# Kernel tuning notes

Hardware: AMD Instinct MI355X
Metric: run time of the kernel (lower is better)

The kernel has to match this reference:

```python
import jax, jax.numpy as jnp
import numpy as np

B, S, E = 4, 2048, 1024
H, D = 16, 64
SCALE = D ** -0.5


def setup_inputs() -> dict:
    key = jax.random.key(0)
    ks = jax.random.split(key, 6)
    x = jax.random.normal(ks[0], (B, S, E), dtype=jnp.float32)
    # per-head projection weights stacked along head axis: [H, E, D]
    Wq = jax.random.normal(ks[1], (H, E, D), dtype=jnp.float32) * 0.02
    Wk = jax.random.normal(ks[2], (H, E, D), dtype=jnp.float32) * 0.02
    Wv = jax.random.normal(ks[3], (H, E, D), dtype=jnp.float32) * 0.02
    # output projection: concat(H*D) -> E, with bias (nn.Linear default)
    Wo = jax.random.normal(ks[4], (H * D, E), dtype=jnp.float32) * 0.02
    bo = jax.random.normal(ks[5], (E,), dtype=jnp.float32) * 0.02
    return {"x": x, "Wq": Wq, "Wk": Wk, "Wv": Wv, "Wo": Wo, "bo": bo}


def reference(x, Wq, Wk, Wv, Wo, bo):
    # batched QKV projections for all heads at once
    q = jnp.einsum('bse,hed->bhsd', x, Wq)
    k = jnp.einsum('bse,hed->bhsd', x, Wk)
    v = jnp.einsum('bse,hed->bhsd', x, Wv)
    # full (non-causal) attention, scores [b,h,s,s]
    scores = jnp.einsum('bhsd,bhtd->bhst', q, k) * SCALE
    attn = jax.nn.softmax(scores, axis=-1)
    o = jnp.einsum('bhst,bhtd->bhsd', attn, v)
    # concat heads in head order along feature dim -> [b,s,H*D]
    o = o.transpose(0, 2, 1, 3).reshape(x.shape[0], x.shape[1], -1)
    return o @ Wo + bo
```

## Files before the change

kernel.cpp:

```cpp
#include <hip/hip_runtime.h>
#include <hip/hip_fp16.h>
#include <stdint.h>

#define BB 4
#define SS 2048
#define EE 1024
#define HH 16
#define DD 64

typedef _Float16 half8 __attribute__((ext_vector_type(8)));
typedef __fp16 fp16x2 __attribute__((ext_vector_type(2)));
typedef float f32x4 __attribute__((ext_vector_type(4)));
typedef float f32x16 __attribute__((ext_vector_type(16)));
typedef uint32_t u32;
typedef uint32_t u32x2 __attribute__((ext_vector_type(2)));

#define MFMA32(a, b, c) __builtin_amdgcn_mfma_f32_16x16x32_f16((a), (b), (c), 0, 0, 0)
#define MFMA3216(a, b, c) __builtin_amdgcn_mfma_f32_32x32x16_f16((a), (b), (c), 0, 0, 0)

#define GLD_LDS16(g, l)                                                        \
  __builtin_amdgcn_global_load_lds(                                            \
      (const __attribute__((address_space(1))) u32*)(const void*)(g),          \
      (__attribute__((address_space(3))) u32*)(void*)(l), 16, 0, 0)

static __device__ __forceinline__ u32 pkh(float a, float b) {
  union { fp16x2 h; u32 u; } z;
  z.h = __builtin_amdgcn_cvt_pkrtz(a, b);
  return z.u;
}

static __device__ __forceinline__ void plswap(u32& a, u32& b) {
  asm("v_permlane32_swap_b32 %0, %1" : "+v"(a), "+v"(b));
}

__global__ __launch_bounds__(256) void conv_x_k(const float* __restrict__ x,
                                                _Float16* __restrict__ xh) {
  size_t i = ((size_t)blockIdx.x * 256 + threadIdx.x) * 8;
  f32x4 a = *(const f32x4*)(x + i);
  f32x4 b = *(const f32x4*)(x + i + 4);
  half8 o;
  o[0] = (_Float16)a[0]; o[1] = (_Float16)a[1];
  o[2] = (_Float16)a[2]; o[3] = (_Float16)a[3];
  o[4] = (_Float16)b[0]; o[5] = (_Float16)b[1];
  o[6] = (_Float16)b[2]; o[7] = (_Float16)b[3];
  *(half8*)(xh + i) = o;
}

__global__ __launch_bounds__(256) void conv_w_k(const float* __restrict__ Wq,
                                                const float* __restrict__ Wk,
                                                const float* __restrict__ Wv,
                                                _Float16* __restrict__ Wt) {
  __shared__ float T[64][65];
  int bid = blockIdx.x;
  int sel = bid >> 8, rem = bid & 255;
  int h = rem >> 4, e0 = (rem & 15) * 64;
  const float* W = (sel == 0 ? Wq : sel == 1 ? Wk : Wv) + (size_t)h * EE * DD;
  float scale = (sel == 0) ? 0.18033688011112042f : 1.0f;
  int tid = threadIdx.x;
  {
    int e = tid >> 2, d0 = (tid & 3) * 16;
#pragma unroll
    for (int i = 0; i < 4; ++i) {
      f32x4 v = *(const f32x4*)(W + (size_t)(e0 + e) * DD + d0 + i * 4);
      T[e][d0 + i * 4 + 0] = v[0];
      T[e][d0 + i * 4 + 1] = v[1];
      T[e][d0 + i * 4 + 2] = v[2];
      T[e][d0 + i * 4 + 3] = v[3];
    }
  }
  __syncthreads();
  {
    int d = tid >> 2, c0 = (tid & 3) * 16;
    half8 o0, o1;
#pragma unroll
    for (int i = 0; i < 8; ++i) o0[i] = (_Float16)(T[c0 + i][d] * scale);
#pragma unroll
    for (int i = 0; i < 8; ++i) o1[i] = (_Float16)(T[c0 + 8 + i][d] * scale);
    _Float16* dst = Wt + ((size_t)sel * 1024 + h * 64 + d) * EE + e0 + c0;
    *(half8*)dst = o0;
    *(half8*)(dst + 8) = o1;
  }
}

__global__ __launch_bounds__(256) void conv_wo_k(const float* __restrict__ Wo,
                                                 _Float16* __restrict__ Wot) {
  __shared__ float T[64][65];
  int bid = blockIdx.x;
  int k0 = (bid >> 4) * 64, n0 = (bid & 15) * 64;
  int tid = threadIdx.x;
  {
    int k = tid >> 2, c0 = (tid & 3) * 16;
#pragma unroll
    for (int i = 0; i < 4; ++i) {
      f32x4 v = *(const f32x4*)(Wo + (size_t)(k0 + k) * EE + n0 + c0 + i * 4);
      T[k][c0 + i * 4 + 0] = v[0];
      T[k][c0 + i * 4 + 1] = v[1];
      T[k][c0 + i * 4 + 2] = v[2];
      T[k][c0 + i * 4 + 3] = v[3];
    }
  }
  __syncthreads();
  {
    int n = tid >> 2, c0 = (tid & 3) * 16;
    half8 o0, o1;
#pragma unroll
    for (int i = 0; i < 8; ++i) o0[i] = (_Float16)T[c0 + i][n];
#pragma unroll
    for (int i = 0; i < 8; ++i) o1[i] = (_Float16)T[c0 + 8 + i][n];
    _Float16* dst = Wot + (size_t)(n0 + n) * EE + k0 + c0;
    *(half8*)dst = o0;
    *(half8*)(dst + 8) = o1;
  }
}

__global__ __launch_bounds__(256) void vtrans_k(const _Float16* __restrict__ v,
                                                _Float16* __restrict__ vT) {
  __shared__ _Float16 T[64][72];
  int bid = blockIdx.x;
  int bh = bid >> 5, st = bid & 31;
  const _Float16* vp = v + (size_t)bh * SS * DD + (size_t)st * 64 * DD;
  _Float16* op = vT + (size_t)bh * DD * SS + (size_t)st * 64;
  int tid = threadIdx.x;
  {
    int r = tid >> 2, c0 = (tid & 3) * 16;
    half8 a = *(const half8*)(vp + (size_t)r * DD + c0);
    half8 b = *(const half8*)(vp + (size_t)r * DD + c0 + 8);
#pragma unroll
    for (int j = 0; j < 8; ++j) T[c0 + j][r] = a[j];
#pragma unroll
    for (int j = 0; j < 8; ++j) T[c0 + 8 + j][r] = b[j];
  }
  __syncthreads();
  {
    int d = tid >> 2, sc = (tid & 3) * 16;
    half8 o0 = *(const half8*)&T[d][sc];
    half8 o1 = *(const half8*)&T[d][sc + 8];
    *(half8*)(op + (size_t)d * SS + sc) = o0;
    *(half8*)(op + (size_t)d * SS + sc + 8) = o1;
  }
}

__global__ __launch_bounds__(256, 3) void qkv_proj_k(
    const _Float16* __restrict__ xh, const _Float16* __restrict__ Wt,
    _Float16* __restrict__ qkv) {
  __shared__ __align__(16) _Float16 As[128 * 32];
  __shared__ __align__(16) _Float16 Bs[128 * 32];
  int bid = blockIdx.x;
  int nblk = bid % 24, mblk = bid / 24;
  int row0 = mblk * 128, n0 = nblk * 128;
  int tid = threadIdx.x, lane = tid & 63, w = tid >> 6;
  int wm = w >> 1, wn = w & 1;
  int l15 = lane & 15, lhi = lane >> 4;

  f32x4 acc[4][4];
#pragma unroll
  for (int i = 0; i < 4; ++i)
#pragma unroll
    for (int j = 0; j < 4; ++j) acc[i][j] = (f32x4){0.f, 0.f, 0.f, 0.f};

  const char* Ab = (const char*)xh + (size_t)row0 * 2048;
  const char* Bb = (const char*)Wt + (size_t)n0 * 2048;
  int ob0 = w * 1024 + lane * 16;

  for (int k0 = 0; k0 < EE; k0 += 32) {
    __syncthreads();
    GLD_LDS16(Ab + (size_t)(ob0 >> 6) * 2048 + k0 * 2 + (ob0 & 63),
              (char*)As + w * 1024);
    GLD_LDS16(Ab + (size_t)((ob0 + 4096) >> 6) * 2048 + k0 * 2 + (ob0 & 63),
              (char*)As + 4096 + w * 1024);
    GLD_LDS16(Bb + (size_t)(ob0 >> 6) * 2048 + k0 * 2 + (ob0 & 63),
              (char*)Bs + w * 1024);
    GLD_LDS16(Bb + (size_t)((ob0 + 4096) >> 6) * 2048 + k0 * 2 + (ob0 & 63),
              (char*)Bs + 4096 + w * 1024);
    __syncthreads();
    half8 a[4], b[4];
#pragma unroll
    for (int mf = 0; mf < 4; ++mf)
      a[mf] = *(const half8*)(As + (wm * 64 + mf * 16 + l15) * 32 + 8 * lhi);
#pragma unroll
    for (int nf = 0; nf < 4; ++nf)
      b[nf] = *(const half8*)(Bs + (wn * 64 + nf * 16 + l15) * 32 + 8 * lhi);
#pragma unroll
    for (int mf = 0; mf < 4; ++mf)
#pragma unroll
      for (int nf = 0; nf < 4; ++nf)
        acc[mf][nf] = MFMA32(a[mf], b[nf], acc[mf][nf]);
  }

  const size_t KOFF = (size_t)BB * HH * SS * DD;
#pragma unroll
  for (int mf = 0; mf < 4; ++mf)
#pragma unroll
    for (int nf = 0; nf < 4; ++nf)
#pragma unroll
      for (int r = 0; r < 4; ++r) {
        int row = row0 + wm * 64 + mf * 16 + 4 * lhi + r;
        int n = n0 + wn * 64 + nf * 16 + l15;
        int sel = n >> 10, hh = (n >> 6) & 15, d = n & 63;
        int b_ = row >> 11, s = row & 2047;
        qkv[(size_t)sel * KOFF + (((size_t)b_ * HH + hh) * SS + s) * DD + d] =
            (_Float16)acc[mf][nf][r];
      }
}

__global__ __launch_bounds__(256, 2) void attn_k(
    const _Float16* __restrict__ qkv, const _Float16* __restrict__ vT,
    _Float16* __restrict__ ob) {
  __shared__ __align__(16) _Float16 Ks[2][64 * 64];
  __shared__ __align__(16) _Float16 Vs[2][64 * 64];

  const int bid = blockIdx.x;
  const int bh = bid >> 3, qb = bid & 7;
  const int b_ = bh >> 4, h = bh & 15;
  const size_t KOFF = (size_t)BB * HH * SS * DD;
  const _Float16* qp = qkv + (size_t)bh * SS * DD;
  const char* kp = (const char*)(qkv + KOFF + (size_t)bh * SS * DD);
  const char* vtp = (const char*)(vT + (size_t)bh * DD * SS);

  const int tid = threadIdx.x, lane = tid & 63, w = tid >> 6;
  const int l31 = lane & 31, u = lane >> 5;
  const int q0 = qb * 256 + w * 64;

  half8 qf[4][2];
#pragma unroll
  for (int ekf = 0; ekf < 4; ++ekf)
#pragma unroll
    for (int nq = 0; nq < 2; ++nq)
      qf[ekf][nq] = *(const half8*)(qp +
          (size_t)(q0 + nq * 32 + l31) * DD + ekf * 16 + u * 8);

  f32x16 oa00 = {}, oa10 = {}, oa01 = {}, oa11 = {};
  float rs0 = 0.f, rs1 = 0.f;

  const int prow = tid >> 3;
  const int pcol = (tid & 7) * 16;
  const int scol = pcol ^ (16 * (prow & 7));
  const int lds0 = tid * 16;
  const int xsw = 16 * (l31 & 7);
  const int NT = SS / 64;

  GLD_LDS16(kp + prow * 128 + scol, (char*)Ks[0] + lds0);
  GLD_LDS16(kp + (prow + 32) * 128 + scol, (char*)Ks[0] + 4096 + lds0);
  GLD_LDS16(vtp + (size_t)prow * 4096 + scol, (char*)Vs[0] + lds0);
  GLD_LDS16(vtp + (size_t)(prow + 32) * 4096 + scol, (char*)Vs[0] + 4096 + lds0);
  __syncthreads();

  for (int it = 0; it < NT; ++it) {
    const int cur = it & 1;
    if (it + 1 < NT) {
      const char* kn = kp + (size_t)(it + 1) * 8192;
      const char* vn = vtp + (size_t)(it + 1) * 128;
      GLD_LDS16(kn + prow * 128 + scol, (char*)Ks[cur ^ 1] + lds0);
      GLD_LDS16(kn + (prow + 32) * 128 + scol, (char*)Ks[cur ^ 1] + 4096 + lds0);
      GLD_LDS16(vn + (size_t)prow * 4096 + scol, (char*)Vs[cur ^ 1] + lds0);
      GLD_LDS16(vn + (size_t)(prow + 32) * 4096 + scol,
                (char*)Vs[cur ^ 1] + 4096 + lds0);
    }
    const char* kb = (const char*)Ks[cur];
    const char* vb = (const char*)Vs[cur];

#pragma unroll
    for (int nt = 0; nt < 2; ++nt) {
      const char* krow = kb + (size_t)(32 * nt + l31) * 128;
      half8 kA0 = *(const half8*)(krow + ((16 * u) ^ xsw));
      half8 kA1 = *(const half8*)(krow + ((32 + 16 * u) ^ xsw));
      half8 kA2 = *(const half8*)(krow + ((64 + 16 * u) ^ xsw));
      half8 kA3 = *(const half8*)(krow + ((96 + 16 * u) ^ xsw));
      f32x16 s0 = {}, s1 = {};
      s0 = MFMA3216(kA0, qf[0][0], s0);
      s1 = MFMA3216(kA0, qf[0][1], s1);
      s0 = MFMA3216(kA1, qf[1][0], s0);
      s1 = MFMA3216(kA1, qf[1][1], s1);
      s0 = MFMA3216(kA2, qf[2][0], s0);
      s1 = MFMA3216(kA2, qf[2][1], s1);
      s0 = MFMA3216(kA3, qf[3][0], s0);
      s1 = MFMA3216(kA3, qf[3][1], s1);

      u32 w0[8], w1[8];
#pragma unroll
      for (int m = 0; m < 8; ++m) {
        float a0 = __builtin_amdgcn_exp2f(s0[2 * m]);
        float a1 = __builtin_amdgcn_exp2f(s0[2 * m + 1]);
        rs0 += a0 + a1;
        w0[m] = pkh(a0, a1);
        float c0 = __builtin_amdgcn_exp2f(s1[2 * m]);
        float c1 = __builtin_amdgcn_exp2f(s1[2 * m + 1]);
        rs1 += c0 + c1;
        w1[m] = pkh(c0, c1);
      }

#pragma unroll
      for (int kfl = 0; kfl < 2; ++kfl) {
        u32 p00 = w0[4 * kfl + 0], p02 = w0[4 * kfl + 2];
        u32 p01 = w0[4 * kfl + 1], p03 = w0[4 * kfl + 3];
        plswap(p00, p02);
        plswap(p01, p03);
        u32 p10 = w1[4 * kfl + 0], p12 = w1[4 * kfl + 2];
        u32 p11 = w1[4 * kfl + 1], p13 = w1[4 * kfl + 3];
        plswap(p10, p12);
        plswap(p11, p13);
        union { u32 q[4]; half8 h; } pb0, pb1;
        pb0.q[0] = p00; pb0.q[1] = p01; pb0.q[2] = p02; pb0.q[3] = p03;
        pb1.q[0] = p10; pb1.q[1] = p11; pb1.q[2] = p12; pb1.q[3] = p13;
        const int kf = 2 * nt + kfl;
        const char* vcol = vb + ((32 * kf + 16 * u) ^ xsw);
        half8 vA0 = *(const half8*)(vcol + (size_t)l31 * 128);
        half8 vA1 = *(const half8*)(vcol + (size_t)(32 + l31) * 128);
        oa00 = MFMA3216(vA0, pb0.h, oa00);
        oa10 = MFMA3216(vA1, pb0.h, oa10);
        oa01 = MFMA3216(vA0, pb1.h, oa01);
        oa11 = MFMA3216(vA1, pb1.h, oa11);
      }
    }
    __syncthreads();
  }

  float inv0 = 1.0f / (rs0 + __shfl_xor(rs0, 32, 64));
  float inv1 = 1.0f / (rs1 + __shfl_xor(rs1, 32, 64));

#define STORE_OA(OA, MD, NQ, INV)                                              \
  {                                                                            \
    _Float16* dst = ob + (size_t)(b_ * SS + q0 + 32 * (NQ) + l31) * 1024 +     \
                    h * 64 + 32 * (MD) + 4 * u;                                \
    _Pragma("unroll")                                                          \
    for (int rr = 0; rr < 4; ++rr) {                                           \
      u32x2 pr;                                                                \
      pr.x = pkh(OA[4 * rr + 0] * (INV), OA[4 * rr + 1] * (INV));              \
      pr.y = pkh(OA[4 * rr + 2] * (INV), OA[4 * rr + 3] * (INV));              \
      *(u32x2*)(dst + 8 * rr) = pr;                                            \
    }                                                                          \
  }
  STORE_OA(oa00, 0, 0, inv0)
  STORE_OA(oa10, 1, 0, inv0)
  STORE_OA(oa01, 0, 1, inv1)
  STORE_OA(oa11, 1, 1, inv1)
#undef STORE_OA
}

__global__ __launch_bounds__(256, 3) void oproj_k(
    const _Float16* __restrict__ ob, const _Float16* __restrict__ Wot,
    const float* __restrict__ bo, float* __restrict__ out) {
  __shared__ __align__(16) _Float16 As[128 * 32];
  __shared__ __align__(16) _Float16 Bs[128 * 32];
  int bid = blockIdx.x;
  int nblk = bid & 7, mblk = bid >> 3;
  int row0 = mblk * 128, n0 = nblk * 128;
  int tid = threadIdx.x, lane = tid & 63, w = tid >> 6;
  int wm = w >> 1, wn = w & 1;
  int l15 = lane & 15, lhi = lane >> 4;

  f32x4 acc[4][4];
#pragma unroll
  for (int i = 0; i < 4; ++i)
#pragma unroll
    for (int j = 0; j < 4; ++j) acc[i][j] = (f32x4){0.f, 0.f, 0.f, 0.f};

  const char* Ab = (const char*)ob + (size_t)row0 * 2048;
  const char* Bb = (const char*)Wot + (size_t)n0 * 2048;
  int ob0 = w * 1024 + lane * 16;

  for (int k0 = 0; k0 < EE; k0 += 32) {
    __syncthreads();
    GLD_LDS16(Ab + (size_t)(ob0 >> 6) * 2048 + k0 * 2 + (ob0 & 63),
              (char*)As + w * 1024);
    GLD_LDS16(Ab + (size_t)((ob0 + 4096) >> 6) * 2048 + k0 * 2 + (ob0 & 63),
              (char*)As + 4096 + w * 1024);
    GLD_LDS16(Bb + (size_t)(ob0 >> 6) * 2048 + k0 * 2 + (ob0 & 63),
              (char*)Bs + w * 1024);
    GLD_LDS16(Bb + (size_t)((ob0 + 4096) >> 6) * 2048 + k0 * 2 + (ob0 & 63),
              (char*)Bs + 4096 + w * 1024);
    __syncthreads();
    half8 a[4], b[4];
#pragma unroll
    for (int mf = 0; mf < 4; ++mf)
      a[mf] = *(const half8*)(As + (wm * 64 + mf * 16 + l15) * 32 + 8 * lhi);
#pragma unroll
    for (int nf = 0; nf < 4; ++nf)
      b[nf] = *(const half8*)(Bs + (wn * 64 + nf * 16 + l15) * 32 + 8 * lhi);
#pragma unroll
    for (int mf = 0; mf < 4; ++mf)
#pragma unroll
      for (int nf = 0; nf < 4; ++nf)
        acc[mf][nf] = MFMA32(a[mf], b[nf], acc[mf][nf]);
  }

#pragma unroll
  for (int mf = 0; mf < 4; ++mf)
#pragma unroll
    for (int nf = 0; nf < 4; ++nf) {
      int n = n0 + wn * 64 + nf * 16 + l15;
      float bias = bo[n];
#pragma unroll
      for (int r = 0; r < 4; ++r) {
        int row = row0 + wm * 64 + mf * 16 + 4 * lhi + r;
        out[(size_t)row * EE + n] = acc[mf][nf][r] + bias;
      }
    }
}

extern "C" void kernel_launch(void* const* d_in, const int* in_sizes, int n_in,
                              void* d_out, int out_size, void* d_ws, size_t ws_size,
                              hipStream_t stream) {
  const float* x  = (const float*)d_in[0];
  const float* Wq = (const float*)d_in[1];
  const float* Wk = (const float*)d_in[2];
  const float* Wv = (const float*)d_in[3];
  const float* Wo = (const float*)d_in[4];
  const float* bo = (const float*)d_in[5];
  float* out = (float*)d_out;

  const size_t KOFF = (size_t)BB * HH * SS * DD;
  _Float16* qkv = (_Float16*)d_ws;
  _Float16* obuf = qkv + 3 * KOFF;
  _Float16* xh = (_Float16*)d_out;
  _Float16* Wt = xh + (size_t)BB * SS * EE;
  _Float16* vTbuf = xh;
  _Float16* Wot = qkv;

  conv_x_k<<<dim3(4096), dim3(256), 0, stream>>>(x, xh);
  conv_w_k<<<dim3(768), dim3(256), 0, stream>>>(Wq, Wk, Wv, Wt);
  qkv_proj_k<<<dim3(64 * 24), dim3(256), 0, stream>>>(xh, Wt, qkv);
  vtrans_k<<<dim3(64 * 32), dim3(256), 0, stream>>>(qkv + 2 * KOFF, vTbuf);
  attn_k<<<dim3(64 * 8), dim3(256), 0, stream>>>(qkv, vTbuf, obuf);
  conv_wo_k<<<dim3(256), dim3(256), 0, stream>>>(Wo, Wot);
  oproj_k<<<dim3(64 * 8), dim3(256), 0, stream>>>(obuf, Wot, bo, out);
}
```

Before: 200.7 us.

## Shrink attention blocks, add XCD-aware block remapping and MFMA priority hints

```diff
diff --git a/kernel.cpp b/kernel.cpp
--- a/kernel.cpp
+++ b/kernel.cpp
@@ -145,7 +145,8 @@
     _Float16* __restrict__ qkv) {
   __shared__ __align__(16) _Float16 As[128 * 32];
   __shared__ __align__(16) _Float16 Bs[128 * 32];
-  int bid = blockIdx.x;
+  int bid0 = blockIdx.x;
+  int bid = (bid0 & 7) * 192 + (bid0 >> 3);
   int nblk = bid % 24, mblk = bid / 24;
   int row0 = mblk * 128, n0 = nblk * 128;
   int tid = threadIdx.x, lane = tid & 63, w = tid >> 6;
@@ -203,14 +204,15 @@
       }
 }
 
-__global__ __launch_bounds__(256, 2) void attn_k(
+__global__ __launch_bounds__(128, 4) void attn_k(
     const _Float16* __restrict__ qkv, const _Float16* __restrict__ vT,
     _Float16* __restrict__ ob) {
   __shared__ __align__(16) _Float16 Ks[2][64 * 64];
   __shared__ __align__(16) _Float16 Vs[2][64 * 64];
 
-  const int bid = blockIdx.x;
-  const int bh = bid >> 3, qb = bid & 7;
+  const int bid0 = blockIdx.x;
+  const int bid = (bid0 & 7) * 128 + (bid0 >> 3);
+  const int bh = bid >> 4, qb = bid & 15;
   const int b_ = bh >> 4, h = bh & 15;
   const size_t KOFF = (size_t)BB * HH * SS * DD;
   const _Float16* qp = qkv + (size_t)bh * SS * DD;
@@ -219,7 +221,7 @@
 
   const int tid = threadIdx.x, lane = tid & 63, w = tid >> 6;
   const int l31 = lane & 31, u = lane >> 5;
-  const int q0 = qb * 256 + w * 64;
+  const int q0 = qb * 128 + w * 64;
 
   half8 qf[4][2];
 #pragma unroll
@@ -232,17 +234,18 @@
   f32x16 oa00 = {}, oa10 = {}, oa01 = {}, oa11 = {};
   float rs0 = 0.f, rs1 = 0.f;
 
-  const int prow = tid >> 3;
-  const int pcol = (tid & 7) * 16;
-  const int scol = pcol ^ (16 * (prow & 7));
+  const int trow = tid >> 3;
+  const int scol = ((tid & 7) * 16) ^ (16 * (trow & 7));
   const int lds0 = tid * 16;
   const int xsw = 16 * (l31 & 7);
   const int NT = SS / 64;
 
-  GLD_LDS16(kp + prow * 128 + scol, (char*)Ks[0] + lds0);
-  GLD_LDS16(kp + (prow + 32) * 128 + scol, (char*)Ks[0] + 4096 + lds0);
-  GLD_LDS16(vtp + (size_t)prow * 4096 + scol, (char*)Vs[0] + lds0);
-  GLD_LDS16(vtp + (size_t)(prow + 32) * 4096 + scol, (char*)Vs[0] + 4096 + lds0);
+#pragma unroll
+  for (int j = 0; j < 4; ++j) {
+    GLD_LDS16(kp + (trow + 16 * j) * 128 + scol, (char*)Ks[0] + j * 2048 + lds0);
+    GLD_LDS16(vtp + (size_t)(trow + 16 * j) * 4096 + scol,
+              (char*)Vs[0] + j * 2048 + lds0);
+  }
   __syncthreads();
 
   for (int it = 0; it < NT; ++it) {
@@ -250,11 +253,13 @@
     if (it + 1 < NT) {
       const char* kn = kp + (size_t)(it + 1) * 8192;
       const char* vn = vtp + (size_t)(it + 1) * 128;
-      GLD_LDS16(kn + prow * 128 + scol, (char*)Ks[cur ^ 1] + lds0);
-      GLD_LDS16(kn + (prow + 32) * 128 + scol, (char*)Ks[cur ^ 1] + 4096 + lds0);
-      GLD_LDS16(vn + (size_t)prow * 4096 + scol, (char*)Vs[cur ^ 1] + lds0);
-      GLD_LDS16(vn + (size_t)(prow + 32) * 4096 + scol,
-                (char*)Vs[cur ^ 1] + 4096 + lds0);
+#pragma unroll
+      for (int j = 0; j < 4; ++j) {
+        GLD_LDS16(kn + (trow + 16 * j) * 128 + scol,
+                  (char*)Ks[cur ^ 1] + j * 2048 + lds0);
+        GLD_LDS16(vn + (size_t)(trow + 16 * j) * 4096 + scol,
+                  (char*)Vs[cur ^ 1] + j * 2048 + lds0);
+      }
     }
     const char* kb = (const char*)Ks[cur];
     const char* vb = (const char*)Vs[cur];
@@ -267,6 +272,7 @@
       half8 kA2 = *(const half8*)(krow + ((64 + 16 * u) ^ xsw));
       half8 kA3 = *(const half8*)(krow + ((96 + 16 * u) ^ xsw));
       f32x16 s0 = {}, s1 = {};
+      __builtin_amdgcn_s_setprio(1);
       s0 = MFMA3216(kA0, qf[0][0], s0);
       s1 = MFMA3216(kA0, qf[0][1], s1);
       s0 = MFMA3216(kA1, qf[1][0], s0);
@@ -275,6 +281,7 @@
       s1 = MFMA3216(kA2, qf[2][1], s1);
       s0 = MFMA3216(kA3, qf[3][0], s0);
       s1 = MFMA3216(kA3, qf[3][1], s1);
+      __builtin_amdgcn_s_setprio(0);
 
       u32 w0[8], w1[8];
 #pragma unroll
@@ -306,10 +313,12 @@
         const char* vcol = vb + ((32 * kf + 16 * u) ^ xsw);
         half8 vA0 = *(const half8*)(vcol + (size_t)l31 * 128);
         half8 vA1 = *(const half8*)(vcol + (size_t)(32 + l31) * 128);
+        __builtin_amdgcn_s_setprio(1);
         oa00 = MFMA3216(vA0, pb0.h, oa00);
         oa10 = MFMA3216(vA1, pb0.h, oa10);
         oa01 = MFMA3216(vA0, pb1.h, oa01);
         oa11 = MFMA3216(vA1, pb1.h, oa11);
+        __builtin_amdgcn_s_setprio(0);
       }
     }
     __syncthreads();
@@ -342,7 +351,8 @@
     const float* __restrict__ bo, float* __restrict__ out) {
   __shared__ __align__(16) _Float16 As[128 * 32];
   __shared__ __align__(16) _Float16 Bs[128 * 32];
-  int bid = blockIdx.x;
+  int bid0 = blockIdx.x;
+  int bid = (bid0 & 7) * 64 + (bid0 >> 3);
   int nblk = bid & 7, mblk = bid >> 3;
   int row0 = mblk * 128, n0 = nblk * 128;
   int tid = threadIdx.x, lane = tid & 63, w = tid >> 6;
@@ -421,7 +431,7 @@
   conv_w_k<<<dim3(768), dim3(256), 0, stream>>>(Wq, Wk, Wv, Wt);
   qkv_proj_k<<<dim3(64 * 24), dim3(256), 0, stream>>>(xh, Wt, qkv);
   vtrans_k<<<dim3(64 * 32), dim3(256), 0, stream>>>(qkv + 2 * KOFF, vTbuf);
-  attn_k<<<dim3(64 * 8), dim3(256), 0, stream>>>(qkv, vTbuf, obuf);
+  attn_k<<<dim3(64 * 16), dim3(128), 0, stream>>>(qkv, vTbuf, obuf);
   conv_wo_k<<<dim3(256), dim3(256), 0, stream>>>(Wo, Wot);
   oproj_k<<<dim3(64 * 8), dim3(256), 0, stream>>>(obuf, Wot, bo, out);
 }
```

After: 210.2 us. 1.05x slower.
